# Performance work log

Hardware: AMD Instinct MI355X
Metric: run time of the kernel (lower is better)

The kernel has to match this reference:

```python
import jax, jax.numpy as jnp
import numpy as np

SIGMA = 0.5
EPS = 1e-7


def _offdiag(M):
    # M: [n, n] -> [n, n-1], row i keeps columns j != i (same order as
    # torch masked_select with (1 - eye) mask followed by view(n, n-1)).
    n = M.shape[0]
    j = jnp.arange(n - 1)
    cols = j[None, :] + (j[None, :] >= jnp.arange(n)[:, None]).astype(j.dtype)  # [n, n-1]
    return jnp.take_along_axis(M, cols, axis=1)


def _pairwise_neg_dist(features):
    # -||f_i - f_j||_2 with a grad-safe sqrt (diagonal is exactly 0; torch's
    # norm backward yields 0 there, so we guard the sqrt).
    diff = features[:, None, :] - features[None, :, :]          # [n, n, d]
    sq = jnp.sum(diff * diff, axis=-1)                          # [n, n]
    safe = jnp.where(sq > 0, sq, 1.0)
    return -jnp.where(sq > 0, jnp.sqrt(safe), 0.0)


def setup_inputs() -> dict:
    key = jax.random.key(0)
    k1, k2 = jax.random.split(key)
    feature = jax.random.normal(k1, (512, 512), dtype=jnp.float32)
    label = jax.random.uniform(k2, (512, 1), dtype=jnp.float32)
    return {"feature": feature, "label": label}


def reference(feature, label):
    n = feature.shape[0]
    # R[i, j] = sum_c |label_i - label_j|
    R = jnp.sum(jnp.abs(label[:, None, :] - label[None, :, :]), axis=-1)  # [n, n]

    F = _pairwise_neg_dist(feature) * SIGMA                               # [n, n]
    F_max = jax.lax.stop_gradient(jnp.max(F, axis=1, keepdims=True))
    F = F - F_max
    scaled_F = jax.nn.softmax(F, axis=1)                                  # [n, n]

    F_off = _offdiag(F)            # [n, n-1]
    S_off = _offdiag(scaled_F)     # [n, n-1]
    R_off = _offdiag(R)            # [n, n-1]

    # neg_mask[k, i, j] = (R_off[i, j] >= R_off[i, k]); here laid out [i, k, j].
    mask = (R_off[:, None, :] >= R_off[:, :, None]).astype(F.dtype)       # [n, n-1, n-1]
    denom = jnp.einsum('ikj,ij->ik', mask, S_off)                         # [n, n-1]

    pos_log_probs = F_off - jnp.log(denom + EPS)                          # [n, n-1]
    loss = -jnp.sum(pos_log_probs) / (n * (n - 1))
    return loss
```

## Files before the change

kernel.cpp:

```cpp
#include <hip/hip_runtime.h>
#include <math.h>

#define N 512
#define SIGMA 0.5f
#define EPS 1e-7f

typedef __attribute__((ext_vector_type(8))) short bf16x8;
typedef __attribute__((ext_vector_type(4))) float f32x4;

__device__ __forceinline__ unsigned short f2bf(float x) {
    unsigned int b = __float_as_uint(x);
    b += 0x7FFFu + ((b >> 16) & 1u);
    return (unsigned short)(b >> 16);
}

__global__ void convert_kernel(const float* __restrict__ feat,
                               unsigned short* __restrict__ featb,
                               float* __restrict__ sqn,
                               float* __restrict__ out) {
    const int row = blockIdx.x;
    const int lane = threadIdx.x;
    if (row == 0 && lane == 0) out[0] = 0.f;

    const float* f = feat + row * N;
    unsigned short* fb = featb + row * N;
    float s = 0.f;
    #pragma unroll
    for (int sweep = 0; sweep < 2; ++sweep) {
        int c = sweep * 256 + lane * 4;
        float4 v = *(const float4*)(f + c);
        unsigned short b0 = f2bf(v.x), b1 = f2bf(v.y), b2 = f2bf(v.z), b3 = f2bf(v.w);
        ushort4 packed = make_ushort4(b0, b1, b2, b3);
        *(ushort4*)(fb + c) = packed;
        float r0 = __uint_as_float((unsigned int)b0 << 16);
        float r1 = __uint_as_float((unsigned int)b1 << 16);
        float r2 = __uint_as_float((unsigned int)b2 << 16);
        float r3 = __uint_as_float((unsigned int)b3 << 16);
        s += r0 * r0 + r1 * r1 + r2 * r2 + r3 * r3;
    }
    #pragma unroll
    for (int off = 32; off > 0; off >>= 1) s += __shfl_down(s, off);
    if (lane == 0) sqn[row] = s;
}

__global__ void fmat_mfma_kernel(const unsigned short* __restrict__ featb,
                                 const float* __restrict__ sqn,
                                 float* __restrict__ Fm) {
    const int r0 = blockIdx.y * 16;
    const int c0 = blockIdx.x * 16;
    const int lane = threadIdx.x;
    const int m = lane & 15;
    const int kb = (lane >> 4) * 8;

    const unsigned short* arow = featb + (size_t)(r0 + m) * N + kb;
    const unsigned short* brow = featb + (size_t)(c0 + m) * N + kb;

    f32x4 acc = {0.f, 0.f, 0.f, 0.f};
    #pragma unroll
    for (int k0 = 0; k0 < N; k0 += 32) {
        bf16x8 a = *(const bf16x8*)(arow + k0);
        bf16x8 b = *(const bf16x8*)(brow + k0);
        acc = __builtin_amdgcn_mfma_f32_16x16x32_bf16(a, b, acc, 0, 0, 0);
    }

    const int col = c0 + (lane & 15);
    const int rowb = r0 + (lane >> 4) * 4;
    const float nc = sqn[col];
    #pragma unroll
    for (int r = 0; r < 4; ++r) {
        const int row = rowb + r;
        float sq = sqn[row] + nc - 2.f * acc[r];
        float v = (row == col) ? 0.f : -SIGMA * sqrtf(fmaxf(sq, 0.f));
        Fm[(size_t)row * N + col] = v;
    }
}

__global__ __launch_bounds__(512, 4)
void row_kernel(const float* __restrict__ Fm,
                const float* __restrict__ label,
                float* __restrict__ out) {
    const int i = blockIdx.x;
    const int t = threadIdx.x;
    const int wave = t >> 6, lane = t & 63;

    __shared__ __align__(16) float Rs[N];
    __shared__ __align__(16) float Ss[N];
    __shared__ float red[8];

    const float li = label[i];
    const float f = Fm[(size_t)i * N + t];
    const float Rk = fabsf(li - label[t]);
    Rs[t] = Rk;

    const float e = __expf(f);

    float s = e;
    #pragma unroll
    for (int off = 32; off > 0; off >>= 1) s += __shfl_xor(s, off);
    if (lane == 0) red[wave] = s;
    __syncthreads();
    const float Z = red[0] + red[1] + red[2] + red[3] +
                    red[4] + red[5] + red[6] + red[7];

    float S = e / Z;
    if (t == i) S = 0.f;
    Ss[t] = S;
    __syncthreads();

    float denom = 0.f;
    const float4* R4 = (const float4*)Rs;
    const float4* S4 = (const float4*)Ss;
    #pragma unroll 16
    for (int j4 = 0; j4 < N / 4; ++j4) {
        float4 r = R4[j4];
        float4 sv = S4[j4];
        denom += (r.x >= Rk) ? sv.x : 0.f;
        denom += (r.y >= Rk) ? sv.y : 0.f;
        denom += (r.z >= Rk) ? sv.z : 0.f;
        denom += (r.w >= Rk) ? sv.w : 0.f;
    }

    float part = (t == i) ? 0.f : (f - __logf(denom + EPS));

    #pragma unroll
    for (int off = 32; off > 0; off >>= 1) part += __shfl_xor(part, off);
    if (lane == 0) red[wave] = part;
    __syncthreads();
    if (t == 0) {
        float tot = red[0] + red[1] + red[2] + red[3] +
                    red[4] + red[5] + red[6] + red[7];
        atomicAdd(out, tot * (-1.f / ((float)N * (float)(N - 1))));
    }
}

extern "C" void kernel_launch(void* const* d_in, const int* in_sizes, int n_in,
                              void* d_out, int out_size, void* d_ws, size_t ws_size,
                              hipStream_t stream) {
    const float* feature = (const float*)d_in[0];
    const float* label   = (const float*)d_in[1];
    float* out = (float*)d_out;

    float* Fm             = (float*)d_ws;
    unsigned short* featb = (unsigned short*)(Fm + (size_t)N * N);
    float* sqn            = (float*)(featb + (size_t)N * N);

    convert_kernel<<<N, 64, 0, stream>>>(feature, featb, sqn, out);
    {
        dim3 grid(N / 16, N / 16);
        fmat_mfma_kernel<<<grid, 64, 0, stream>>>(featb, sqn, Fm);
    }
    row_kernel<<<N, N, 0, stream>>>(Fm, label, out);
}
```

Before: 78.10 us.

## Replace O(n^2) per-row mask sum with label sort plus prefix-sum binary search

Labels are sorted once by rank-counting in an extra block of the setup kernel, which also takes over the bf16 conversion using 8 rows per block. In the row kernel, each row builds a prefix sum of softmax weights in sorted-label order. Each thread then finds the set of j with |l_i - l_j| >= R_k by binary searching the contiguous interval of distances below R_k around position i. This replaces the 512-step shared-memory scan per thread with O(log n) work, in exchange for extra scans, barriers and gathered reads.

```diff
diff --git a/kernel.cpp b/kernel.cpp
--- a/kernel.cpp
+++ b/kernel.cpp
@@ -14,33 +14,57 @@
     return (unsigned short)(b >> 16);
 }
 
-__global__ void convert_kernel(const float* __restrict__ feat,
-                               unsigned short* __restrict__ featb,
-                               float* __restrict__ sqn,
-                               float* __restrict__ out) {
-    const int row = blockIdx.x;
-    const int lane = threadIdx.x;
-    if (row == 0 && lane == 0) out[0] = 0.f;
-
-    const float* f = feat + row * N;
-    unsigned short* fb = featb + row * N;
-    float s = 0.f;
-    #pragma unroll
-    for (int sweep = 0; sweep < 2; ++sweep) {
-        int c = sweep * 256 + lane * 4;
-        float4 v = *(const float4*)(f + c);
-        unsigned short b0 = f2bf(v.x), b1 = f2bf(v.y), b2 = f2bf(v.z), b3 = f2bf(v.w);
-        ushort4 packed = make_ushort4(b0, b1, b2, b3);
-        *(ushort4*)(fb + c) = packed;
-        float r0 = __uint_as_float((unsigned int)b0 << 16);
-        float r1 = __uint_as_float((unsigned int)b1 << 16);
-        float r2 = __uint_as_float((unsigned int)b2 << 16);
-        float r3 = __uint_as_float((unsigned int)b3 << 16);
-        s += r0 * r0 + r1 * r1 + r2 * r2 + r3 * r3;
+__global__ __launch_bounds__(512)
+void setup_kernel(const float* __restrict__ feat,
+                  const float* __restrict__ label,
+                  unsigned short* __restrict__ featb,
+                  float* __restrict__ sqn,
+                  float* __restrict__ sl, int* __restrict__ sidx,
+                  int* __restrict__ ipos, float* __restrict__ out) {
+    const int t = threadIdx.x;
+    if (blockIdx.x < 64) {
+        const int wave = t >> 6, lane = t & 63;
+        const int row = blockIdx.x * 8 + wave;
+        const float* f = feat + (size_t)row * N;
+        unsigned short* fb = featb + (size_t)row * N;
+        float s = 0.f;
+        #pragma unroll
+        for (int sweep = 0; sweep < 2; ++sweep) {
+            int c = sweep * 256 + lane * 4;
+            float4 v = *(const float4*)(f + c);
+            unsigned short b0 = f2bf(v.x), b1 = f2bf(v.y),
+                           b2 = f2bf(v.z), b3 = f2bf(v.w);
+            *(ushort4*)(fb + c) = make_ushort4(b0, b1, b2, b3);
+            float r0 = __uint_as_float((unsigned int)b0 << 16);
+            float r1 = __uint_as_float((unsigned int)b1 << 16);
+            float r2 = __uint_as_float((unsigned int)b2 << 16);
+            float r3 = __uint_as_float((unsigned int)b3 << 16);
+            s += r0 * r0 + r1 * r1 + r2 * r2 + r3 * r3;
+        }
+        #pragma unroll
+        for (int off = 32; off > 0; off >>= 1) s += __shfl_down(s, off);
+        if (lane == 0) sqn[row] = s;
+    } else {
+        __shared__ __align__(16) float lab[N];
+        const float lt = label[t];
+        lab[t] = lt;
+        if (t == 0) out[0] = 0.f;
+        __syncthreads();
+        int rank = 0;
+        const float4* L4 = (const float4*)lab;
+        #pragma unroll 8
+        for (int j4 = 0; j4 < N / 4; ++j4) {
+            float4 v = L4[j4];
+            int j = j4 * 4;
+            rank += ((v.x < lt) || (v.x == lt && (j + 0) < t)) ? 1 : 0;
+            rank += ((v.y < lt) || (v.y == lt && (j + 1) < t)) ? 1 : 0;
+            rank += ((v.z < lt) || (v.z == lt && (j + 2) < t)) ? 1 : 0;
+            rank += ((v.w < lt) || (v.w == lt && (j + 3) < t)) ? 1 : 0;
+        }
+        sl[rank] = lt;
+        sidx[rank] = t;
+        ipos[t] = rank;
     }
-    #pragma unroll
-    for (int off = 32; off > 0; off >>= 1) s += __shfl_down(s, off);
-    if (lane == 0) sqn[row] = s;
 }
 
 __global__ void fmat_mfma_kernel(const unsigned short* __restrict__ featb,
@@ -75,51 +99,69 @@
     }
 }
 
-__global__ __launch_bounds__(512, 4)
+__global__ __launch_bounds__(512)
 void row_kernel(const float* __restrict__ Fm,
                 const float* __restrict__ label,
+                const float* __restrict__ sl,
+                const int* __restrict__ sidx,
+                const int* __restrict__ ipos,
                 float* __restrict__ out) {
     const int i = blockIdx.x;
     const int t = threadIdx.x;
     const int wave = t >> 6, lane = t & 63;
 
-    __shared__ __align__(16) float Rs[N];
+    __shared__ __align__(16) float ds_[N];
     __shared__ __align__(16) float Ss[N];
+    __shared__ __align__(16) float Ps[N];
     __shared__ float red[8];
+    __shared__ float wsum[8];
 
     const float li = label[i];
     const float f = Fm[(size_t)i * N + t];
-    const float Rk = fabsf(li - label[t]);
-    Rs[t] = Rk;
-
     const float e = __expf(f);
 
-    float s = e;
+    ds_[t] = fabsf(li - sl[t]);
+
+    float z = e;
     #pragma unroll
-    for (int off = 32; off > 0; off >>= 1) s += __shfl_xor(s, off);
-    if (lane == 0) red[wave] = s;
+    for (int off = 32; off > 0; off >>= 1) z += __shfl_xor(z, off);
+    if (lane == 0) red[wave] = z;
     __syncthreads();
     const float Z = red[0] + red[1] + red[2] + red[3] +
                     red[4] + red[5] + red[6] + red[7];
-
     float S = e / Z;
     if (t == i) S = 0.f;
     Ss[t] = S;
     __syncthreads();
 
-    float denom = 0.f;
-    const float4* R4 = (const float4*)Rs;
-    const float4* S4 = (const float4*)Ss;
-    #pragma unroll 16
-    for (int j4 = 0; j4 < N / 4; ++j4) {
-        float4 r = R4[j4];
-        float4 sv = S4[j4];
-        denom += (r.x >= Rk) ? sv.x : 0.f;
-        denom += (r.y >= Rk) ? sv.y : 0.f;
-        denom += (r.z >= Rk) ? sv.z : 0.f;
-        denom += (r.w >= Rk) ? sv.w : 0.f;
+    float v = Ss[sidx[t]];
+    #pragma unroll
+    for (int off = 1; off < 64; off <<= 1) {
+        float u = __shfl_up(v, off);
+        if (lane >= off) v += u;
     }
+    if (lane == 63) wsum[wave] = v;
+    __syncthreads();
+    float base = 0.f;
+    #pragma unroll
+    for (int w = 0; w < 8; ++w) base += (w < wave) ? wsum[w] : 0.f;
+    Ps[t] = base + v;
+    __syncthreads();
 
+    const float total = Ps[N - 1];
+    const int posi = ipos[i];
+    const int pt = ipos[t];
+    const float Rk = ds_[pt];
+
+    int lo = 0, hi = posi + 1;
+    while (lo < hi) { int mid = (lo + hi) >> 1; if (ds_[mid] < Rk) hi = mid; else lo = mid + 1; }
+    const int La = lo;
+    lo = posi; hi = N;
+    while (lo < hi) { int mid = (lo + hi) >> 1; if (ds_[mid] >= Rk) hi = mid; else lo = mid + 1; }
+    const int Rb = lo - 1;
+
+    const float inner = ((Rb >= 0) ? Ps[Rb] : 0.f) - ((La > 0) ? Ps[La - 1] : 0.f);
+    const float denom = total - inner;
     float part = (t == i) ? 0.f : (f - __logf(denom + EPS));
 
     #pragma unroll
@@ -143,11 +185,15 @@
     float* Fm             = (float*)d_ws;
     unsigned short* featb = (unsigned short*)(Fm + (size_t)N * N);
     float* sqn            = (float*)(featb + (size_t)N * N);
+    float* sl             = sqn + N;
+    int*   sidx           = (int*)(sl + N);
+    int*   ipos           = sidx + N;
 
-    convert_kernel<<<N, 64, 0, stream>>>(feature, featb, sqn, out);
+    setup_kernel<<<65, 512, 0, stream>>>(feature, label, featb, sqn,
+                                         sl, sidx, ipos, out);
     {
         dim3 grid(N / 16, N / 16);
         fmat_mfma_kernel<<<grid, 64, 0, stream>>>(featb, sqn, Fm);
     }
-    row_kernel<<<N, N, 0, stream>>>(Fm, label, out);
+    row_kernel<<<N, N, 0, stream>>>(Fm, label, sl, sidx, ipos, out);
 }
```

New measurement: 87.37 us. 1.12x slower.

## Fuse convert, distance GEMM and row loss into one cooperative kernel

Applied to the files above, without the earlier changes.

Replaces the three-kernel pipeline with a single cooperative kernel of 256 blocks, each owning two rows. The kernel converts features to bf16 and computes squared norms, does a grid-wide sync, then builds its F rows in LDS via MFMA before doing the softmax and rank-denominator work. This drops the global F matrix round trip and two kernel launches. The cost is redundant MFMA work, since each half-block computes a full 16-row slab but keeps one row, plus every block rereading all of featb from L2 and the overhead of a grid barrier.

```diff
diff --git a/kernel.cpp b/kernel.cpp
--- a/kernel.cpp
+++ b/kernel.cpp
@@ -1,5 +1,8 @@
 #include <hip/hip_runtime.h>
+#include <hip/hip_cooperative_groups.h>
 #include <math.h>
+
+namespace cg = cooperative_groups;
 
 #define N 512
 #define SIGMA 0.5f
@@ -13,124 +16,138 @@
     b += 0x7FFFu + ((b >> 16) & 1u);
     return (unsigned short)(b >> 16);
 }
-
-__global__ void convert_kernel(const float* __restrict__ feat,
-                               unsigned short* __restrict__ featb,
-                               float* __restrict__ sqn,
-                               float* __restrict__ out) {
-    const int row = blockIdx.x;
-    const int lane = threadIdx.x;
-    if (row == 0 && lane == 0) out[0] = 0.f;
-
-    const float* f = feat + row * N;
-    unsigned short* fb = featb + row * N;
-    float s = 0.f;
-    #pragma unroll
-    for (int sweep = 0; sweep < 2; ++sweep) {
-        int c = sweep * 256 + lane * 4;
-        float4 v = *(const float4*)(f + c);
-        unsigned short b0 = f2bf(v.x), b1 = f2bf(v.y), b2 = f2bf(v.z), b3 = f2bf(v.w);
-        ushort4 packed = make_ushort4(b0, b1, b2, b3);
-        *(ushort4*)(fb + c) = packed;
-        float r0 = __uint_as_float((unsigned int)b0 << 16);
-        float r1 = __uint_as_float((unsigned int)b1 << 16);
-        float r2 = __uint_as_float((unsigned int)b2 << 16);
-        float r3 = __uint_as_float((unsigned int)b3 << 16);
-        s += r0 * r0 + r1 * r1 + r2 * r2 + r3 * r3;
-    }
-    #pragma unroll
-    for (int off = 32; off > 0; off >>= 1) s += __shfl_down(s, off);
-    if (lane == 0) sqn[row] = s;
+__device__ __forceinline__ float bf2f(unsigned short h) {
+    return __uint_as_float((unsigned int)h << 16);
 }
 
-__global__ void fmat_mfma_kernel(const unsigned short* __restrict__ featb,
-                                 const float* __restrict__ sqn,
-                                 float* __restrict__ Fm) {
-    const int r0 = blockIdx.y * 16;
-    const int c0 = blockIdx.x * 16;
-    const int lane = threadIdx.x;
-    const int m = lane & 15;
-    const int kb = (lane >> 4) * 8;
-
-    const unsigned short* arow = featb + (size_t)(r0 + m) * N + kb;
-    const unsigned short* brow = featb + (size_t)(c0 + m) * N + kb;
-
-    f32x4 acc = {0.f, 0.f, 0.f, 0.f};
-    #pragma unroll
-    for (int k0 = 0; k0 < N; k0 += 32) {
-        bf16x8 a = *(const bf16x8*)(arow + k0);
-        bf16x8 b = *(const bf16x8*)(brow + k0);
-        acc = __builtin_amdgcn_mfma_f32_16x16x32_bf16(a, b, acc, 0, 0, 0);
-    }
-
-    const int col = c0 + (lane & 15);
-    const int rowb = r0 + (lane >> 4) * 4;
-    const float nc = sqn[col];
-    #pragma unroll
-    for (int r = 0; r < 4; ++r) {
-        const int row = rowb + r;
-        float sq = sqn[row] + nc - 2.f * acc[r];
-        float v = (row == col) ? 0.f : -SIGMA * sqrtf(fmaxf(sq, 0.f));
-        Fm[(size_t)row * N + col] = v;
-    }
-}
-
-__global__ __launch_bounds__(512, 4)
-void row_kernel(const float* __restrict__ Fm,
-                const float* __restrict__ label,
-                float* __restrict__ out) {
-    const int i = blockIdx.x;
+__global__ __launch_bounds__(512, 2)
+void fused_kernel(const float* __restrict__ feat,
+                  const float* __restrict__ label,
+                  unsigned short* __restrict__ featb,
+                  float* __restrict__ sqn,
+                  float* __restrict__ out) {
+    const int b = blockIdx.x;
     const int t = threadIdx.x;
     const int wave = t >> 6, lane = t & 63;
 
+    __shared__ __align__(16) float FrowA[N];
+    __shared__ __align__(16) float FrowB[N];
     __shared__ __align__(16) float Rs[N];
     __shared__ __align__(16) float Ss[N];
-    __shared__ float red[8];
+    __shared__ float red0[8], red1[8];
 
-    const float li = label[i];
-    const float f = Fm[(size_t)i * N + t];
-    const float Rk = fabsf(li - label[t]);
-    Rs[t] = Rk;
+    const int rA = b, rB = b + 256;
 
-    const float e = __expf(f);
+    {
+        float v0 = feat[(size_t)rA * N + t];
+        float v1 = feat[(size_t)rB * N + t];
+        unsigned short h0 = f2bf(v0), h1 = f2bf(v1);
+        featb[(size_t)rA * N + t] = h0;
+        featb[(size_t)rB * N + t] = h1;
+        float q0 = bf2f(h0); q0 *= q0;
+        float q1 = bf2f(h1); q1 *= q1;
+        #pragma unroll
+        for (int off = 32; off > 0; off >>= 1) {
+            q0 += __shfl_xor(q0, off);
+            q1 += __shfl_xor(q1, off);
+        }
+        if (lane == 0) { red0[wave] = q0; red1[wave] = q1; }
+        __syncthreads();
+        if (t == 0) {
+            float s0 = 0.f, s1 = 0.f;
+            #pragma unroll
+            for (int w = 0; w < 8; ++w) { s0 += red0[w]; s1 += red1[w]; }
+            sqn[rA] = s0; sqn[rB] = s1;
+            if (b == 0) out[0] = 0.f;
+        }
+    }
+    __threadfence();
+    cg::this_grid().sync();
 
-    float s = e;
-    #pragma unroll
-    for (int off = 32; off > 0; off >>= 1) s += __shfl_xor(s, off);
-    if (lane == 0) red[wave] = s;
-    __syncthreads();
-    const float Z = red[0] + red[1] + red[2] + red[3] +
-                    red[4] + red[5] + red[6] + red[7];
+    {
+        const int rl = b & 15;
+        const int slab = (wave < 4) ? (rA & ~15) : ((rB & ~15));
+        float* Frow = (wave < 4) ? FrowA : FrowB;
+        const int w4 = wave & 3;
+        const int m = lane & 15;
+        const int kb = (lane >> 4) * 8;
 
-    float S = e / Z;
-    if (t == i) S = 0.f;
-    Ss[t] = S;
-    __syncthreads();
+        const unsigned short* abase = featb + (size_t)(slab + m) * N + kb;
+        bf16x8 afr[16];
+        #pragma unroll
+        for (int k0 = 0; k0 < 16; ++k0)
+            afr[k0] = *(const bf16x8*)(abase + k0 * 32);
 
-    float denom = 0.f;
-    const float4* R4 = (const float4*)Rs;
-    const float4* S4 = (const float4*)Ss;
-    #pragma unroll 16
-    for (int j4 = 0; j4 < N / 4; ++j4) {
-        float4 r = R4[j4];
-        float4 sv = S4[j4];
-        denom += (r.x >= Rk) ? sv.x : 0.f;
-        denom += (r.y >= Rk) ? sv.y : 0.f;
-        denom += (r.z >= Rk) ? sv.z : 0.f;
-        denom += (r.w >= Rk) ? sv.w : 0.f;
+        #pragma unroll
+        for (int j = 0; j < 8; ++j) {
+            const int c0 = (w4 + j * 4) * 16;
+            const unsigned short* bbase = featb + (size_t)(c0 + m) * N + kb;
+            f32x4 acc = {0.f, 0.f, 0.f, 0.f};
+            #pragma unroll
+            for (int k0 = 0; k0 < 16; ++k0) {
+                bf16x8 bfr = *(const bf16x8*)(bbase + k0 * 32);
+                acc = __builtin_amdgcn_mfma_f32_16x16x32_bf16(afr[k0], bfr, acc, 0, 0, 0);
+            }
+            if ((lane >> 4) == (rl >> 2))
+                Frow[c0 + m] = acc[rl & 3];
+        }
+        __syncthreads();
     }
 
-    float part = (t == i) ? 0.f : (f - __logf(denom + EPS));
+    float blocksum = 0.f;
+    #pragma unroll 1
+    for (int rr = 0; rr < 2; ++rr) {
+        const int i = (rr == 0) ? rA : rB;
+        const float* Frow = (rr == 0) ? FrowA : FrowB;
+        const float li = label[i];
+        const float sqi = sqn[i];
 
-    #pragma unroll
-    for (int off = 32; off > 0; off >>= 1) part += __shfl_xor(part, off);
-    if (lane == 0) red[wave] = part;
-    __syncthreads();
-    if (t == 0) {
-        float tot = red[0] + red[1] + red[2] + red[3] +
-                    red[4] + red[5] + red[6] + red[7];
-        atomicAdd(out, tot * (-1.f / ((float)N * (float)(N - 1))));
+        const float dotc = Frow[t];
+        const float sqc = sqn[t];
+        const float F = (t == i) ? 0.f
+                      : -SIGMA * sqrtf(fmaxf(sqi + sqc - 2.f * dotc, 0.f));
+        const float Rk = fabsf(li - label[t]);
+        Rs[t] = Rk;
+        const float e = __expf(F);
+
+        float z = e;
+        #pragma unroll
+        for (int off = 32; off > 0; off >>= 1) z += __shfl_xor(z, off);
+        if (lane == 0) red0[wave] = z;
+        __syncthreads();
+        const float Z = red0[0] + red0[1] + red0[2] + red0[3] +
+                        red0[4] + red0[5] + red0[6] + red0[7];
+        float S = e / Z;
+        if (t == i) S = 0.f;
+        Ss[t] = S;
+        __syncthreads();
+
+        float denom = 0.f;
+        const float4* R4 = (const float4*)Rs;
+        const float4* S4 = (const float4*)Ss;
+        #pragma unroll 8
+        for (int j4 = 0; j4 < N / 4; ++j4) {
+            float4 r = R4[j4];
+            float4 sv = S4[j4];
+            denom += (r.x >= Rk) ? sv.x : 0.f;
+            denom += (r.y >= Rk) ? sv.y : 0.f;
+            denom += (r.z >= Rk) ? sv.z : 0.f;
+            denom += (r.w >= Rk) ? sv.w : 0.f;
+        }
+
+        float part = (t == i) ? 0.f : (F - __logf(denom + EPS));
+        #pragma unroll
+        for (int off = 32; off > 0; off >>= 1) part += __shfl_xor(part, off);
+        if (lane == 0) red1[wave] = part;
+        __syncthreads();
+        if (t == 0) {
+            blocksum += red1[0] + red1[1] + red1[2] + red1[3] +
+                        red1[4] + red1[5] + red1[6] + red1[7];
+        }
+        __syncthreads();
     }
+    if (t == 0)
+        atomicAdd(out, blocksum * (-1.f / ((float)N * (float)(N - 1))));
 }
 
 extern "C" void kernel_launch(void* const* d_in, const int* in_sizes, int n_in,
@@ -140,14 +157,11 @@
     const float* label   = (const float*)d_in[1];
     float* out = (float*)d_out;
 
-    float* Fm             = (float*)d_ws;
-    unsigned short* featb = (unsigned short*)(Fm + (size_t)N * N);
-    float* sqn            = (float*)(featb + (size_t)N * N);
+    unsigned short* featb = (unsigned short*)d_ws;
+    float* sqn = (float*)((char*)d_ws + (size_t)N * N * sizeof(unsigned short));
 
-    convert_kernel<<<N, 64, 0, stream>>>(feature, featb, sqn, out);
-    {
-        dim3 grid(N / 16, N / 16);
-        fmat_mfma_kernel<<<grid, 64, 0, stream>>>(featb, sqn, Fm);
-    }
-    row_kernel<<<N, N, 0, stream>>>(Fm, label, out);
+    void* args[] = { (void*)&feature, (void*)&label, (void*)&featb,
+                     (void*)&sqn, (void*)&out };
+    hipLaunchCooperativeKernel((const void*)fused_kernel,
+                               dim3(256), dim3(512), args, 0, stream);
 }
```

New measurement: 186.8 us. 139% more time.
